# Performance work log

Measured on AMD Instinct MI355X. Metric: run time of the kernel, lower is better.

The kernel has to match this reference:

```python
import jax, jax.numpy as jnp
import numpy as np

K = 3  # kernel size (hardcoded in module defaults; padding=1, stride=1, dilation=1)


def conv2d(x, w, b, pad=1):
    # x: [B,C,H,W], w: [O,C,kh,kw]
    out = jax.lax.conv_general_dilated(
        x, w, window_strides=(1, 1), padding=[(pad, pad), (pad, pad)],
        dimension_numbers=("NCHW", "OIHW", "NCHW"))
    return out + b[None, :, None, None]


def _bilinear_sample(img, py, px):
    # img: [C,H,W]; py, px: [K*K,Ho,Wo] float sample coords.
    # Zero-padded bilinear sampling (matches torchvision deform_conv2d):
    # each of the 4 corner taps contributes 0 if it lies outside the image.
    H, W = img.shape[1], img.shape[2]
    y0 = jnp.floor(py)
    x0 = jnp.floor(px)
    y1, x1 = y0 + 1.0, x0 + 1.0
    wy1 = py - y0
    wy0 = 1.0 - wy1
    wx1 = px - x0
    wx0 = 1.0 - wx1

    def corner(y, x):
        yi = jnp.clip(y.astype(jnp.int32), 0, H - 1)
        xi = jnp.clip(x.astype(jnp.int32), 0, W - 1)
        valid = ((y >= 0) & (y <= H - 1) & (x >= 0) & (x <= W - 1))
        return img[:, yi, xi] * valid.astype(img.dtype)[None]  # [C,K*K,Ho,Wo]

    return (corner(y0, x0) * (wy0 * wx0)[None]
            + corner(y0, x1) * (wy0 * wx1)[None]
            + corner(y1, x0) * (wy1 * wx0)[None]
            + corner(y1, x1) * (wy1 * wx1)[None])


def setup_inputs() -> dict:
    key = jax.random.key(0)
    ks = jax.random.split(key, 4)
    B, C, O, H, W = 8, 128, 256, 96, 96
    x = jax.random.normal(ks[0], (B, C, H, W), dtype=jnp.float32)
    # scale offset/mask conv weights so learned offsets stay a few pixels
    offset_w = jax.random.normal(ks[1], (2 * K * K, C, K, K), dtype=jnp.float32) * 0.01
    offset_b = jnp.zeros((2 * K * K,), dtype=jnp.float32)
    mask_w = jax.random.normal(ks[2], (K * K, C, K, K), dtype=jnp.float32) * 0.05
    mask_b = jnp.zeros((K * K,), dtype=jnp.float32)
    weight = jax.random.normal(ks[3], (O, C, K, K), dtype=jnp.float32) * 0.05
    bias = jnp.zeros((O,), dtype=jnp.float32)
    return {"x": x, "offset_w": offset_w, "offset_b": offset_b,
            "mask_w": mask_w, "mask_b": mask_b, "weight": weight, "bias": bias}


def reference(x, offset_w, offset_b, mask_w, mask_b, weight, bias):
    B, C, H, W = x.shape
    O = weight.shape[0]
    pad = 1
    offset = conv2d(x, offset_w, offset_b, pad)              # [B,2*K*K,H,W]
    mask = jax.nn.sigmoid(conv2d(x, mask_w, mask_b, pad))    # [B,K*K,H,W]
    Ho, Wo = offset.shape[2], offset.shape[3]

    # base sampling grid: output pixel - pad + kernel tap position
    kh, kw = jnp.meshgrid(jnp.arange(K), jnp.arange(K), indexing="ij")
    kh = kh.reshape(-1).astype(x.dtype)  # [K*K]
    kw = kw.reshape(-1).astype(x.dtype)
    base_y = (jnp.arange(Ho, dtype=x.dtype)[None, :, None] - pad
              + kh[:, None, None])                           # [K*K,Ho,1]
    base_x = (jnp.arange(Wo, dtype=x.dtype)[None, None, :] - pad
              + kw[:, None, None])                           # [K*K,1,Wo]

    # torchvision layout: channel 2k = y-offset, 2k+1 = x-offset for tap k
    off = offset.reshape(B, K * K, 2, Ho, Wo)
    py = base_y[None] + off[:, :, 0]                         # [B,K*K,Ho,Wo]
    px = base_x[None] + off[:, :, 1]

    samples = jax.vmap(_bilinear_sample)(x, py, px)          # [B,C,K*K,Ho,Wo]
    w_flat = weight.reshape(O, C, K * K)
    out = jnp.einsum("bckhw,bkhw,ock->bohw", samples, mask, w_flat)
    return out + bias[None, :, None, None]
```

## Files before the change

kernel.cpp:

```cpp
#include <hip/hip_runtime.h>

#define CIN 128
#define COUT 256
#define IH 96
#define IW 96
#define NB 8
#define HW (IH*IW)
#define NPIX (NB*HW)
#define AST 136
#define BLK_PER_IMG (HW/64)

typedef __attribute__((ext_vector_type(8))) short short8;
typedef __attribute__((ext_vector_type(4))) float floatx4;

static __device__ __forceinline__ short f2bf(float f) {
  unsigned int u = __builtin_bit_cast(unsigned int, f);
  u = u + 0x7fffu + ((u >> 16) & 1u);
  return (short)(u >> 16);
}
static __device__ __forceinline__ float bf2f(short s) {
  unsigned int u = ((unsigned int)(unsigned short)s) << 16;
  return __builtin_bit_cast(float, u);
}

__global__ void prep_weights(const float* __restrict__ weight,
                             const float* __restrict__ offset_w,
                             const float* __restrict__ mask_w,
                             short* __restrict__ Bt2f,
                             short* __restrict__ Bt1f) {
  int idx = blockIdx.x * 256 + threadIdx.x;
  const int n2 = 9 * 4 * 16 * 512;
  if (idx < n2) {
    int e = idx & 7, lane = (idx >> 3) & 63;
    int g = idx >> 9;
    int nl = g & 15, kq = (g >> 4) & 3, tap = g >> 6;
    int o = nl * 16 + (lane & 15);
    int c = kq * 32 + (lane >> 4) * 8 + e;
    Bt2f[idx] = f2bf(weight[(o * CIN + c) * 9 + tap]);
  } else {
    int j = idx - n2;
    if (j < 9 * 4 * 2 * 512) {
      int e = j & 7, lane = (j >> 3) & 63;
      int g = j >> 9;
      int nl = g & 1, kq = (g >> 1) & 3, tap = g >> 3;
      int n = nl * 16 + (lane & 15);
      int c = kq * 32 + (lane >> 4) * 8 + e;
      float v = 0.f;
      if (n < 27)
        v = (n < 18) ? offset_w[(n * CIN + c) * 9 + tap]
                     : mask_w[((n - 18) * CIN + c) * 9 + tap];
      Bt1f[j] = f2bf(v);
    }
  }
}

__global__ __launch_bounds__(256, 8)
void transpose_x(const float* __restrict__ x, short* __restrict__ xt) {
  __shared__ short tile[64 * 130];
  const int tid = threadIdx.x;
  const int lane = tid & 63;
  const int wv = tid >> 6;
  const int p0 = blockIdx.x * 64;
  const int b = p0 / HW;
  const int hw0 = p0 % HW;
  const float* xb = x + (size_t)b * CIN * HW + hw0;

  #pragma unroll
  for (int i = 0; i < 32; ++i) {
    int c = wv + i * 4;
    tile[lane * 130 + c] = f2bf(xb[(size_t)c * HW + lane]);
  }
  __syncthreads();

  unsigned int* dst = (unsigned int*)(xt + ((size_t)b * HW + hw0) * 128);
  #pragma unroll
  for (int i = 0; i < 16; ++i) {
    int idx = i * 256 + tid;
    int px = idx >> 6, cw = idx & 63;
    unsigned int lo = (unsigned short)tile[px * 130 + 2 * cw];
    unsigned int hi = (unsigned short)tile[px * 130 + 2 * cw + 1];
    dst[idx] = lo | (hi << 16);
  }
}

__global__ __launch_bounds__(256, 8)
void offmask_kernel(const short* __restrict__ xt,
                    const short* __restrict__ Bt1f,
                    const float* __restrict__ offset_b,
                    const float* __restrict__ mask_b,
                    float* __restrict__ pmt) {
  const int tid  = threadIdx.x;
  const int lane = tid & 63;
  const int wv   = tid >> 6;
  const int q    = lane >> 4;
  const int m    = lane & 15;
  const int blk  = blockIdx.x;
  const int l    = (blk & 7) * BLK_PER_IMG + (blk >> 3);
  const int p0   = l * 64;
  const int b    = p0 / HW;
  const int p    = p0 + wv * 16 + m;
  const int hw   = p % HW;
  const int h    = hw / IW, w_ = hw % IW;
  const short* xtb = xt + (size_t)b * HW * 128;

  floatx4 acc0 = (floatx4){0.f, 0.f, 0.f, 0.f};
  floatx4 acc1 = (floatx4){0.f, 0.f, 0.f, 0.f};

  for (int tap = 0; tap < 9; ++tap) {
    const int kh = tap / 3, kw = tap % 3;
    const int iy = h + kh - 1, ix = w_ + kw - 1;
    const bool vald = (iy >= 0 && iy < IH && ix >= 0 && ix < IW);
    const size_t pbase = vald ? (size_t)(iy * IW + ix) * 128 : 0;
    #pragma unroll
    for (int kq = 0; kq < 4; ++kq) {
      short8 a = *(const short8*)(xtb + pbase + kq * 32 + q * 8);
      if (!vald) a = (short8){0, 0, 0, 0, 0, 0, 0, 0};
      const short8* b0 = (const short8*)(Bt1f + (size_t)((tap * 4 + kq) * 2 + 0) * 512 + lane * 8);
      const short8* b1 = (const short8*)(Bt1f + (size_t)((tap * 4 + kq) * 2 + 1) * 512 + lane * 8);
      acc0 = __builtin_amdgcn_mfma_f32_16x16x32_bf16(a, *b0, acc0, 0, 0, 0);
      acc1 = __builtin_amdgcn_mfma_f32_16x16x32_bf16(a, *b1, acc1, 0, 0, 0);
    }
  }

  #pragma unroll
  for (int nl = 0; nl < 2; ++nl) {
    floatx4 ac = nl ? acc1 : acc0;
    int ch = nl * 16 + m;
    if (ch < 18) {
      int tap = ch >> 1, plane = ch & 1;
      float cb = offset_b[ch];
      #pragma unroll
      for (int r = 0; r < 4; ++r) {
        int pp = p0 + wv * 16 + q * 4 + r;
        int hwp = pp % HW;
        float base = plane ? (float)(hwp % IW + tap % 3 - 1)
                           : (float)(hwp / IW + tap / 3 - 1);
        pmt[(size_t)(plane * 9 + tap) * NPIX + pp] = ac[r] + cb + base;
      }
    } else if (ch < 27) {
      int tap = ch - 18;
      float cb = mask_b[tap];
      #pragma unroll
      for (int r = 0; r < 4; ++r) {
        int pp = p0 + wv * 16 + q * 4 + r;
        float v = ac[r] + cb;
        pmt[(size_t)(18 + tap) * NPIX + pp] = 1.f / (1.f + expf(-v));
      }
    }
  }
}

__global__ __launch_bounds__(256, 3)
void deform_main(const short* __restrict__ xt,
                 const short* __restrict__ Bt2f,
                 const float* __restrict__ pmt,
                 const float* __restrict__ bias,
                 float* __restrict__ out) {
  __shared__ short Ald[2][64 * AST];

  const int tid  = threadIdx.x;
  const int lane = tid & 63;
  const int wv   = tid >> 6;
  const int q    = lane >> 4;
  const int m    = lane & 15;
  const int blk  = blockIdx.x;
  const int l    = (blk & 7) * BLK_PER_IMG + (blk >> 3);
  const int p0   = l * 64;
  const int b    = p0 / HW;
  const short* xtb = xt + (size_t)b * HW * 128;

  const int spx = lane;
  const int p_s = p0 + spx;
  const int choff = wv * 32;

  floatx4 acc[4][4];
  #pragma unroll
  for (int i = 0; i < 4; ++i)
    #pragma unroll
    for (int j = 0; j < 4; ++j) acc[i][j] = (floatx4){0.f, 0.f, 0.f, 0.f};

  auto stage_tap = [&](int t, short* buf) {
    float py = pmt[(size_t)t * NPIX + p_s];
    float px = pmt[(size_t)(9 + t) * NPIX + p_s];
    float mk = pmt[(size_t)(18 + t) * NPIX + p_s];
    float y0f = floorf(py), x0f = floorf(px);
    float wy1 = py - y0f, wx1 = px - x0f;
    float wy0 = 1.f - wy1, wx0 = 1.f - wx1;
    bool vy0 = (y0f >= 0.f) && (y0f <= (float)(IH - 1));
    bool vy1 = (y0f + 1.f >= 0.f) && (y0f + 1.f <= (float)(IH - 1));
    bool vx0 = (x0f >= 0.f) && (x0f <= (float)(IW - 1));
    bool vx1 = (x0f + 1.f >= 0.f) && (x0f + 1.f <= (float)(IW - 1));
    int iy0 = min(max((int)y0f, 0), IH - 1);
    int iy1 = min(max((int)y0f + 1, 0), IH - 1);
    int ix0 = min(max((int)x0f, 0), IW - 1);
    int ix1 = min(max((int)x0f + 1, 0), IW - 1);
    float w00 = wy0 * wx0 * mk * ((vy0 && vx0) ? 1.f : 0.f);
    float w01 = wy0 * wx1 * mk * ((vy0 && vx1) ? 1.f : 0.f);
    float w10 = wy1 * wx0 * mk * ((vy1 && vx0) ? 1.f : 0.f);
    float w11 = wy1 * wx1 * mk * ((vy1 && vx1) ? 1.f : 0.f);
    const short* r00 = xtb + (size_t)(iy0 * IW + ix0) * 128 + choff;
    const short* r01 = xtb + (size_t)(iy0 * IW + ix1) * 128 + choff;
    const short* r10 = xtb + (size_t)(iy1 * IW + ix0) * 128 + choff;
    const short* r11 = xtb + (size_t)(iy1 * IW + ix1) * 128 + choff;
    short* dst = buf + spx * AST + choff;
    #pragma unroll
    for (int i = 0; i < 4; ++i) {
      short8 s00 = *(const short8*)(r00 + i * 8);
      short8 s01 = *(const short8*)(r01 + i * 8);
      short8 s10 = *(const short8*)(r10 + i * 8);
      short8 s11 = *(const short8*)(r11 + i * 8);
      short8 o;
      #pragma unroll
      for (int j = 0; j < 8; ++j) {
        float v = w00 * bf2f(s00[j]) + w01 * bf2f(s01[j])
                + w10 * bf2f(s10[j]) + w11 * bf2f(s11[j]);
        o[j] = f2bf(v);
      }
      *(short8*)(dst + i * 8) = o;
    }
  };

  stage_tap(0, Ald[0]);
  __syncthreads();

  for (int tap = 0; tap < 9; ++tap) {
    const short* bufr = Ald[tap & 1];
    #pragma unroll
    for (int kq = 0; kq < 4; ++kq) {
      short8 af[4];
      #pragma unroll
      for (int mt = 0; mt < 4; ++mt)
        af[mt] = *(const short8*)(bufr + (mt * 16 + m) * AST + kq * 32 + q * 8);
      short8 bf[4];
      #pragma unroll
      for (int nl = 0; nl < 4; ++nl)
        bf[nl] = *(const short8*)(Bt2f + (size_t)((tap * 4 + kq) * 16 + wv * 4 + nl) * 512 + lane * 8);
      #pragma unroll
      for (int mt = 0; mt < 4; ++mt)
        #pragma unroll
        for (int nl = 0; nl < 4; ++nl)
          acc[mt][nl] = __builtin_amdgcn_mfma_f32_16x16x32_bf16(af[mt], bf[nl], acc[mt][nl], 0, 0, 0);
    }
    if (tap < 8) stage_tap(tap + 1, Ald[(tap + 1) & 1]);
    __syncthreads();
  }

  const int hw0 = p0 % HW;
  #pragma unroll
  for (int nl = 0; nl < 4; ++nl) {
    const int o = wv * 64 + nl * 16 + m;
    const float bs = bias[o];
    float* op = out + (size_t)(b * COUT + o) * HW + hw0;
    #pragma unroll
    for (int mt = 0; mt < 4; ++mt) {
      floatx4 v = acc[mt][nl];
      v[0] += bs; v[1] += bs; v[2] += bs; v[3] += bs;
      *(floatx4*)(op + mt * 16 + q * 4) = v;
    }
  }
}

extern "C" void kernel_launch(void* const* d_in, const int* in_sizes, int n_in,
                              void* d_out, int out_size, void* d_ws, size_t ws_size,
                              hipStream_t stream) {
  const float* x        = (const float*)d_in[0];
  const float* offset_w = (const float*)d_in[1];
  const float* offset_b = (const float*)d_in[2];
  const float* mask_w   = (const float*)d_in[3];
  const float* mask_b   = (const float*)d_in[4];
  const float* weight   = (const float*)d_in[5];
  const float* bias     = (const float*)d_in[6];
  float* out = (float*)d_out;

  char* ws = (char*)d_ws;
  const size_t XT_BYTES  = (size_t)NPIX * 128 * 2;
  const size_t PMT_BYTES = (size_t)27 * NPIX * 4;
  const size_t BT2_BYTES = (size_t)9 * 4 * 16 * 512 * 2;
  short* xtp  = (short*)ws;
  float* pmt  = (float*)(ws + XT_BYTES);
  short* Bt2f = (short*)(ws + XT_BYTES + PMT_BYTES);
  short* Bt1f = (short*)(ws + XT_BYTES + PMT_BYTES + BT2_BYTES);

  prep_weights<<<dim3(1296), dim3(256), 0, stream>>>(weight, offset_w, mask_w, Bt2f, Bt1f);
  transpose_x<<<dim3(NPIX / 64), dim3(256), 0, stream>>>(x, xtp);
  offmask_kernel<<<dim3(NPIX / 64), dim3(256), 0, stream>>>(xtp, Bt1f, offset_b, mask_b, pmt);
  deform_main<<<dim3(NPIX / 64), dim3(256), 0, stream>>>(xtp, Bt2f, pmt, bias, out);
}
```

Measured before the change: 266.8 us.

## Interleave deformable gather with MFMA loop, swizzle LDS, prefetch offsets

The main kernel now spreads the bilinear gather for the next tap across the MFMA k-steps of the current tap, issuing the global corner loads one step ahead and writing the interpolated chunk to LDS afterward. Offsets and mask values are prefetched one extra tap ahead, and LDS rows use an XOR swizzle on 16-byte chunks to cut bank conflicts. The offset/mask conv kernel batches its A/B loads ahead of its MFMAs and lowers its occupancy hint. The aim is to hide gather latency behind matrix math, at the cost of more live registers.

Measured after the change: 257.8 us. -3.4%, faster.

```diff
diff --git a/kernel.cpp b/kernel.cpp
--- a/kernel.cpp
+++ b/kernel.cpp
@@ -21,6 +21,49 @@
 static __device__ __forceinline__ float bf2f(short s) {
   unsigned int u = ((unsigned int)(unsigned short)s) << 16;
   return __builtin_bit_cast(float, u);
+}
+
+struct Corner {
+  float w00, w01, w10, w11;
+  const short *r00, *r01, *r10, *r11;
+};
+
+static __device__ __forceinline__ Corner corner_setup(float py, float px, float mk,
+                                                      const short* xtb, int choff) {
+  Corner c;
+  float y0f = floorf(py), x0f = floorf(px);
+  float wy1 = py - y0f, wx1 = px - x0f;
+  float wy0 = 1.f - wy1, wx0 = 1.f - wx1;
+  bool vy0 = (y0f >= 0.f) && (y0f <= (float)(IH - 1));
+  bool vy1 = (y0f + 1.f >= 0.f) && (y0f + 1.f <= (float)(IH - 1));
+  bool vx0 = (x0f >= 0.f) && (x0f <= (float)(IW - 1));
+  bool vx1 = (x0f + 1.f >= 0.f) && (x0f + 1.f <= (float)(IW - 1));
+  int iy0 = min(max((int)y0f, 0), IH - 1);
+  int iy1 = min(max((int)y0f + 1, 0), IH - 1);
+  int ix0 = min(max((int)x0f, 0), IW - 1);
+  int ix1 = min(max((int)x0f + 1, 0), IW - 1);
+  c.w00 = wy0 * wx0 * mk * ((vy0 && vx0) ? 1.f : 0.f);
+  c.w01 = wy0 * wx1 * mk * ((vy0 && vx1) ? 1.f : 0.f);
+  c.w10 = wy1 * wx0 * mk * ((vy1 && vx0) ? 1.f : 0.f);
+  c.w11 = wy1 * wx1 * mk * ((vy1 && vx1) ? 1.f : 0.f);
+  c.r00 = xtb + (size_t)(iy0 * IW + ix0) * 128 + choff;
+  c.r01 = xtb + (size_t)(iy0 * IW + ix1) * 128 + choff;
+  c.r10 = xtb + (size_t)(iy1 * IW + ix0) * 128 + choff;
+  c.r11 = xtb + (size_t)(iy1 * IW + ix1) * 128 + choff;
+  return c;
+}
+
+static __device__ __forceinline__ short8 interp8(short8 s00, short8 s01,
+                                                 short8 s10, short8 s11,
+                                                 const Corner& c) {
+  short8 o;
+  #pragma unroll
+  for (int j = 0; j < 8; ++j) {
+    float v = c.w00 * bf2f(s00[j]) + c.w01 * bf2f(s01[j])
+            + c.w10 * bf2f(s10[j]) + c.w11 * bf2f(s11[j]);
+    o[j] = f2bf(v);
+  }
+  return o;
 }
 
 __global__ void prep_weights(const float* __restrict__ weight,
@@ -83,7 +126,7 @@
   }
 }
 
-__global__ __launch_bounds__(256, 8)
+__global__ __launch_bounds__(256, 4)
 void offmask_kernel(const short* __restrict__ xt,
                     const short* __restrict__ Bt1f,
                     const float* __restrict__ offset_b,
@@ -111,14 +154,22 @@
     const int iy = h + kh - 1, ix = w_ + kw - 1;
     const bool vald = (iy >= 0 && iy < IH && ix >= 0 && ix < IW);
     const size_t pbase = vald ? (size_t)(iy * IW + ix) * 128 : 0;
+
+    short8 a[4], bb0[4], bb1[4];
+    #pragma unroll
+    for (int kq = 0; kq < 4; ++kq)
+      a[kq] = *(const short8*)(xtb + pbase + kq * 32 + q * 8);
     #pragma unroll
     for (int kq = 0; kq < 4; ++kq) {
-      short8 a = *(const short8*)(xtb + pbase + kq * 32 + q * 8);
-      if (!vald) a = (short8){0, 0, 0, 0, 0, 0, 0, 0};
-      const short8* b0 = (const short8*)(Bt1f + (size_t)((tap * 4 + kq) * 2 + 0) * 512 + lane * 8);
-      const short8* b1 = (const short8*)(Bt1f + (size_t)((tap * 4 + kq) * 2 + 1) * 512 + lane * 8);
-      acc0 = __builtin_amdgcn_mfma_f32_16x16x32_bf16(a, *b0, acc0, 0, 0, 0);
-      acc1 = __builtin_amdgcn_mfma_f32_16x16x32_bf16(a, *b1, acc1, 0, 0, 0);
+      bb0[kq] = *(const short8*)(Bt1f + (size_t)((tap * 4 + kq) * 2 + 0) * 512 + lane * 8);
+      bb1[kq] = *(const short8*)(Bt1f + (size_t)((tap * 4 + kq) * 2 + 1) * 512 + lane * 8);
+    }
+    #pragma unroll
+    for (int kq = 0; kq < 4; ++kq) {
+      short8 av = a[kq];
+      if (!vald) av = (short8){0, 0, 0, 0, 0, 0, 0, 0};
+      acc0 = __builtin_amdgcn_mfma_f32_16x16x32_bf16(av, bb0[kq], acc0, 0, 0, 0);
+      acc1 = __builtin_amdgcn_mfma_f32_16x16x32_bf16(av, bb1[kq], acc1, 0, 0, 0);
     }
   }
 
@@ -169,9 +220,13 @@
   const int b    = p0 / HW;
   const short* xtb = xt + (size_t)b * HW * 128;
 
-  const int spx = lane;
-  const int p_s = p0 + spx;
+  const int spx   = lane;
+  const int p_s   = p0 + spx;
   const int choff = wv * 32;
+  const int wsw   = spx & 3;
+  const int rsw   = m & 3;
+  short* const myrow0 = &Ald[0][spx * AST];
+  short* const myrow1 = &Ald[1][spx * AST];
 
   floatx4 acc[4][4];
   #pragma unroll
@@ -179,70 +234,69 @@
     #pragma unroll
     for (int j = 0; j < 4; ++j) acc[i][j] = (floatx4){0.f, 0.f, 0.f, 0.f};
 
-  auto stage_tap = [&](int t, short* buf) {
-    float py = pmt[(size_t)t * NPIX + p_s];
-    float px = pmt[(size_t)(9 + t) * NPIX + p_s];
-    float mk = pmt[(size_t)(18 + t) * NPIX + p_s];
-    float y0f = floorf(py), x0f = floorf(px);
-    float wy1 = py - y0f, wx1 = px - x0f;
-    float wy0 = 1.f - wy1, wx0 = 1.f - wx1;
-    bool vy0 = (y0f >= 0.f) && (y0f <= (float)(IH - 1));
-    bool vy1 = (y0f + 1.f >= 0.f) && (y0f + 1.f <= (float)(IH - 1));
-    bool vx0 = (x0f >= 0.f) && (x0f <= (float)(IW - 1));
-    bool vx1 = (x0f + 1.f >= 0.f) && (x0f + 1.f <= (float)(IW - 1));
-    int iy0 = min(max((int)y0f, 0), IH - 1);
-    int iy1 = min(max((int)y0f + 1, 0), IH - 1);
-    int ix0 = min(max((int)x0f, 0), IW - 1);
-    int ix1 = min(max((int)x0f + 1, 0), IW - 1);
-    float w00 = wy0 * wx0 * mk * ((vy0 && vx0) ? 1.f : 0.f);
-    float w01 = wy0 * wx1 * mk * ((vy0 && vx1) ? 1.f : 0.f);
-    float w10 = wy1 * wx0 * mk * ((vy1 && vx0) ? 1.f : 0.f);
-    float w11 = wy1 * wx1 * mk * ((vy1 && vx1) ? 1.f : 0.f);
-    const short* r00 = xtb + (size_t)(iy0 * IW + ix0) * 128 + choff;
-    const short* r01 = xtb + (size_t)(iy0 * IW + ix1) * 128 + choff;
-    const short* r10 = xtb + (size_t)(iy1 * IW + ix0) * 128 + choff;
-    const short* r11 = xtb + (size_t)(iy1 * IW + ix1) * 128 + choff;
-    short* dst = buf + spx * AST + choff;
+  {
+    float py = pmt[p_s];
+    float px = pmt[(size_t)9 * NPIX + p_s];
+    float mk = pmt[(size_t)18 * NPIX + p_s];
+    Corner c = corner_setup(py, px, mk, xtb, choff);
     #pragma unroll
     for (int i = 0; i < 4; ++i) {
-      short8 s00 = *(const short8*)(r00 + i * 8);
-      short8 s01 = *(const short8*)(r01 + i * 8);
-      short8 s10 = *(const short8*)(r10 + i * 8);
-      short8 s11 = *(const short8*)(r11 + i * 8);
-      short8 o;
-      #pragma unroll
-      for (int j = 0; j < 8; ++j) {
-        float v = w00 * bf2f(s00[j]) + w01 * bf2f(s01[j])
-                + w10 * bf2f(s10[j]) + w11 * bf2f(s11[j]);
-        o[j] = f2bf(v);
-      }
-      *(short8*)(dst + i * 8) = o;
-    }
-  };
-
-  stage_tap(0, Ald[0]);
+      short8 s00 = *(const short8*)(c.r00 + i * 8);
+      short8 s01 = *(const short8*)(c.r01 + i * 8);
+      short8 s10 = *(const short8*)(c.r10 + i * 8);
+      short8 s11 = *(const short8*)(c.r11 + i * 8);
+      *(short8*)(myrow0 + ((wv * 4 + i) ^ wsw) * 8) = interp8(s00, s01, s10, s11, c);
+    }
+  }
+  float pyN = pmt[(size_t)1 * NPIX + p_s];
+  float pxN = pmt[(size_t)10 * NPIX + p_s];
+  float mkN = pmt[(size_t)19 * NPIX + p_s];
   __syncthreads();
 
   for (int tap = 0; tap < 9; ++tap) {
     const short* bufr = Ald[tap & 1];
+    short* const roww = (tap & 1) ? myrow0 : myrow1;
+    const bool nxt = (tap < 8);
+
+    Corner c;
+    if (nxt) c = corner_setup(pyN, pxN, mkN, xtb, choff);
+    if (tap < 7) {
+      pyN = pmt[(size_t)(tap + 2) * NPIX + p_s];
+      pxN = pmt[(size_t)(tap + 11) * NPIX + p_s];
+      mkN = pmt[(size_t)(tap + 20) * NPIX + p_s];
+    }
+
+    short8 gp00, gp01, gp10, gp11;
     #pragma unroll
     for (int kq = 0; kq < 4; ++kq) {
-      short8 af[4];
-      #pragma unroll
-      for (int mt = 0; mt < 4; ++mt)
-        af[mt] = *(const short8*)(bufr + (mt * 16 + m) * AST + kq * 32 + q * 8);
       short8 bf[4];
       #pragma unroll
       for (int nl = 0; nl < 4; ++nl)
         bf[nl] = *(const short8*)(Bt2f + (size_t)((tap * 4 + kq) * 16 + wv * 4 + nl) * 512 + lane * 8);
+      short8 g00, g01, g10, g11;
+      if (nxt) {
+        g00 = *(const short8*)(c.r00 + kq * 8);
+        g01 = *(const short8*)(c.r01 + kq * 8);
+        g10 = *(const short8*)(c.r10 + kq * 8);
+        g11 = *(const short8*)(c.r11 + kq * 8);
+      }
+      short8 af[4];
+      #pragma unroll
+      for (int mt = 0; mt < 4; ++mt)
+        af[mt] = *(const short8*)(bufr + (mt * 16 + m) * AST + ((kq * 4 + q) ^ rsw) * 8);
       #pragma unroll
       for (int mt = 0; mt < 4; ++mt)
         #pragma unroll
         for (int nl = 0; nl < 4; ++nl)
           acc[mt][nl] = __builtin_amdgcn_mfma_f32_16x16x32_bf16(af[mt], bf[nl], acc[mt][nl], 0, 0, 0);
-    }
-    if (tap < 8) stage_tap(tap + 1, Ald[(tap + 1) & 1]);
-    __syncthreads();
+      if (nxt && kq > 0)
+        *(short8*)(roww + ((wv * 4 + kq - 1) ^ wsw) * 8) = interp8(gp00, gp01, gp10, gp11, c);
+      gp00 = g00; gp01 = g01; gp10 = g10; gp11 = g11;
+    }
+    if (nxt) {
+      *(short8*)(roww + ((wv * 4 + 3) ^ wsw) * 8) = interp8(gp00, gp01, gp10, gp11, c);
+      __syncthreads();
+    }
   }
 
   const int hw0 = p0 % HW;
```
